# Kernel optimization log

Measured on AMD Instinct MI355X. Metric: run time of the kernel, lower is better.

## Reference

```python
import jax, jax.numpy as jnp
import numpy as np

TOPK = 1024
C = 32
FC0 = 256
EPS_BN = 1e-5
EPS_NORM = 1e-12


def setup_inputs() -> dict:
    key = jax.random.key(0)
    ks = jax.random.split(key, 8)
    B, L = 128, 16384
    N = B * L
    x = jax.random.normal(ks[0], (N, C), dtype=jnp.float32)
    length = jnp.full((B,), L, dtype=jnp.int32)
    # conv1d_1: Conv1d(32, 1, 1) -> weight [1, 32, 1] ~ vector [32], bias [1]
    w_att = jax.random.normal(ks[1], (C,), dtype=jnp.float32) * (1.0 / np.sqrt(C))
    b_att = jnp.zeros((1,), dtype=jnp.float32)
    # bn_1: BatchNorm1d(1) (eval mode: use running stats)
    g1 = jnp.ones((1,), dtype=jnp.float32)
    be1 = jnp.zeros((1,), dtype=jnp.float32)
    rm1 = jnp.zeros((1,), dtype=jnp.float32)
    rv1 = jnp.ones((1,), dtype=jnp.float32)
    # fc_1: Linear(TOPK*C, FC0)
    fan_in = TOPK * C
    W_fc = jax.random.normal(ks[2], (FC0, fan_in), dtype=jnp.float32) * (1.0 / np.sqrt(fan_in))
    b_fc = jnp.zeros((FC0,), dtype=jnp.float32)
    # bn_2: BatchNorm1d(FC0) (eval mode)
    g2 = jnp.ones((FC0,), dtype=jnp.float32)
    be2 = jnp.zeros((FC0,), dtype=jnp.float32)
    rm2 = jnp.zeros((FC0,), dtype=jnp.float32)
    rv2 = jnp.ones((FC0,), dtype=jnp.float32)
    return {"x": x, "length": length, "w_att": w_att, "b_att": b_att,
            "g1": g1, "be1": be1, "rm1": rm1, "rv1": rv1,
            "W_fc": W_fc, "b_fc": b_fc,
            "g2": g2, "be2": be2, "rm2": rm2, "rv2": rv2}


def reference(x, length, w_att, b_att, g1, be1, rm1, rv1, W_fc, b_fc, g2, be2, rm2, rv2):
    B = length.shape[0]
    N = x.shape[0]
    L = N // B  # equal-length segments (sum(length) == N)
    # attention score: 1x1 conv over channels + BatchNorm1d(1) (eval)
    att = x @ w_att + b_att[0]                                   # [N]
    att = (att - rm1[0]) * (g1[0] / jnp.sqrt(rv1[0] + EPS_BN)) + be1[0]
    # per-segment descending sort + take top TOPK == top_k per segment
    att_b = att.reshape(B, L)                                    # [B, L]
    x_b = x.reshape(B, L, C)                                     # [B, L, C]
    _, idx = jax.lax.top_k(att_b, TOPK)                          # [B, TOPK]
    ranked = jnp.take_along_axis(x_b, idx[:, :, None], axis=1)   # [B, TOPK, C]
    flat = ranked.reshape(B, TOPK * C)                           # [B, TOPK*C]
    # fc_1 + bn_2 (eval) + L2 row-normalize
    out = flat @ W_fc.T + b_fc                                   # [B, FC0]
    out = (out - rm2) * (g2 / jnp.sqrt(rv2 + EPS_BN)) + be2
    nrm = jnp.maximum(jnp.linalg.norm(out, axis=1, keepdims=True), EPS_NORM)
    return out / nrm
```

## Files before the change

kernel.cpp:

```cpp
#include <hip/hip_runtime.h>
#include <stdint.h>

#define CC 32
#define TOPK 1024
#define FC0 256
#define HL 8192

typedef __attribute__((ext_vector_type(8))) short bf16x8;
typedef __attribute__((ext_vector_type(4))) float f32x4;

__device__ __forceinline__ ushort f2bf(float f) {
    uint32_t u = __float_as_uint(f);
    uint32_t r = u + 0x7FFFu + ((u >> 16) & 1u);
    return (ushort)(r >> 16);
}

__device__ __forceinline__ uint64_t cex(uint64_t v, int s, bool up, int t)
{
    uint64_t o = (uint64_t)__shfl_xor((unsigned long long)v, s, 64);
    bool left = ((t & s) == 0);
    uint64_t mn = v < o ? v : o;
    uint64_t mx = v < o ? o : v;
    return (left == up) ? mn : mx;
}

__global__ __launch_bounds__(256)
void k_att(const float* __restrict__ x,
           const float* __restrict__ w_att, const float* __restrict__ b_att,
           uint32_t* __restrict__ key, int N)
{
    __shared__ float tile[256][CC + 1];
    const int t = threadIdx.x;
    const size_t base = (size_t)blockIdx.x * 256;
    const float4* xv = (const float4*)(x + base * CC);
    #pragma unroll
    for (int i = 0; i < 8; ++i) {
        int e = i * 256 + t;
        float4 v = xv[e];
        int r = e >> 3, c4 = (e & 7) * 4;
        tile[r][c4 + 0] = v.x; tile[r][c4 + 1] = v.y;
        tile[r][c4 + 2] = v.z; tile[r][c4 + 3] = v.w;
    }
    __syncthreads();
    float p[8];
    #pragma unroll
    for (int j = 0; j < 8; ++j) {
        float pj = __fmul_rn(tile[t][j], w_att[j]);
        pj = __fmaf_rn(tile[t][8 + j],  w_att[8 + j],  pj);
        pj = __fmaf_rn(tile[t][16 + j], w_att[16 + j], pj);
        pj = __fmaf_rn(tile[t][24 + j], w_att[24 + j], pj);
        p[j] = pj;
    }
    float q0 = __fadd_rn(p[0], p[1]);
    float q1 = __fadd_rn(p[2], p[3]);
    float q2 = __fadd_rn(p[4], p[5]);
    float q3 = __fadd_rn(p[6], p[7]);
    float dot = __fadd_rn(__fadd_rn(q0, q1), __fadd_rn(q2, q3));
    float v = __fadd_rn(dot, b_att[0]);
    uint32_t bits = __float_as_uint(v);
    key[base + t] = (bits & 0x80000000u) ? ~bits : (bits | 0x80000000u);
}

__global__ __launch_bounds__(1024)
void k_halfsel(const uint32_t* __restrict__ key, uint64_t* __restrict__ cand)
{
    __shared__ uint32_t kv[HL];
    __shared__ uint64_t cv[2048];
    __shared__ uint32_t hist[257];
    __shared__ uint32_t s_prefix, s_k, s_cnt;
    const int t = threadIdx.x;
    const int b = blockIdx.x;
    const int lane = t & 63;
    const uint32_t halfbase = (uint32_t)(b & 1) * HL;

    {
        const uint4* ks = (const uint4*)(key + (size_t)b * HL);
        uint4 a = ks[t], c = ks[t + 1024];
        *(uint4*)&kv[t * 4] = a;
        *(uint4*)&kv[(t + 1024) * 4] = c;
    }
    if (t == 0) { s_prefix = 0; s_k = TOPK; s_cnt = 0; }
    __syncthreads();

    #pragma unroll
    for (int round = 0; round < 2; ++round) {
        if (t < 257) hist[t] = 0;
        __syncthreads();
        const uint32_t pref = s_prefix;
        const uint32_t k = s_k;
        for (int i = t; i < HL; i += 1024) {
            uint32_t u = kv[i];
            if (round == 0) atomicAdd(&hist[u >> 24], 1u);
            else if ((u >> 24) == pref) atomicAdd(&hist[(u >> 16) & 255u], 1u);
        }
        __syncthreads();
        if (t < 64) {
            int l = t;
            uint32_t h0 = hist[4*l], h1 = hist[4*l+1], h2 = hist[4*l+2], h3 = hist[4*l+3];
            uint32_t s3 = h3, s2 = h2 + s3, s1 = h1 + s2, s0 = h0 + s1;
            uint32_t tot = s0, run = tot;
            #pragma unroll
            for (int off = 1; off < 64; off <<= 1) {
                int src = l + off < 64 ? l + off : 63;
                uint32_t o = __shfl(run, src, 64);
                if (l + off < 64) run += o;
            }
            uint32_t esuf = run - tot;
            hist[4*l]   = s0 + esuf; hist[4*l+1] = s1 + esuf;
            hist[4*l+2] = s2 + esuf; hist[4*l+3] = s3 + esuf;
        }
        __syncthreads();
        if (t < 256) {
            uint32_t st = hist[t], sn = hist[t + 1];
            if (st >= k && sn < k) {
                s_prefix = (pref << 8) | (uint32_t)t;
                s_k = k - sn;
            }
        }
        __syncthreads();
    }
    const uint32_t T = s_prefix << 16;

    for (int i = t; i < HL; i += 1024) {
        bool q = kv[i] >= T;
        unsigned long long m = __ballot(q);
        uint32_t base = 0;
        if (lane == 0 && m)
            base = atomicAdd(&s_cnt, (uint32_t)__popcll(m));
        base = __shfl(base, 0);
        if (q) {
            uint32_t pos = base + (uint32_t)__popcll(m & ((1ULL << lane) - 1ULL));
            if (pos < 2048)
                cv[pos] = ((uint64_t)kv[i] << 32)
                        | (uint64_t)(uint32_t)(~(halfbase + (uint32_t)i));
        }
    }
    __syncthreads();
    const uint32_t mm = s_cnt < 2048u ? s_cnt : 2048u;
    for (int i = t; i < 2048; i += 1024)
        if ((uint32_t)i >= mm) cv[i] = 0ULL;
    __syncthreads();

    {
        uint64_t r0 = cv[t], r1 = cv[t + 1024];
        #pragma unroll
        for (int size = 2; size <= 64; size <<= 1) {
            bool up = ((t & size) == 0);
            #pragma unroll
            for (int s = size >> 1; s > 0; s >>= 1) {
                r0 = cex(r0, s, up, t);
                r1 = cex(r1, s, up, t);
            }
        }
        cv[t] = r0; cv[t + 1024] = r1;
    }
    #pragma unroll
    for (int size = 128; size <= 2048; size <<= 1) {
        for (int s = size >> 1; s >= 64; s >>= 1) {
            __syncthreads();
            int i = ((t & ~(s - 1)) << 1) | (t & (s - 1));
            int j = i | s;
            uint64_t va = cv[i], vb = cv[j];
            bool up = ((i & size) == 0);
            if (up ? (va > vb) : (va < vb)) { cv[i] = vb; cv[j] = va; }
        }
        __syncthreads();
        {
            uint64_t a0 = cv[t], a1 = cv[t + 1024];
            bool up0, up1;
            if (size <= 512)      { up0 = ((t & size) == 0); up1 = up0; }
            else if (size == 1024){ up0 = true;  up1 = false; }
            else                  { up0 = true;  up1 = true;  }
            #pragma unroll
            for (int s = 32; s > 0; s >>= 1) {
                a0 = cex(a0, s, up0, t);
                a1 = cex(a1, s, up1, t);
            }
            cv[t] = a0; cv[t + 1024] = a1;
        }
        __syncthreads();
    }
    cand[(size_t)b * TOPK + t] = cv[2047 - t];
}

__global__ __launch_bounds__(1024)
void k_merge(const uint64_t* __restrict__ cand, int* __restrict__ idx_out)
{
    __shared__ uint64_t cv[2048];
    const int t = threadIdx.x;
    const int seg = blockIdx.x;
    cv[t]        = cand[(size_t)(seg * 2) * TOPK + t];
    cv[1024 + t] = cand[(size_t)(seg * 2 + 1) * TOPK + (1023 - t)];
    __syncthreads();
    for (int s = 1024; s >= 1; s >>= 1) {
        int i = ((t & ~(s - 1)) << 1) | (t & (s - 1));
        int j = i | s;
        uint64_t va = cv[i], vb = cv[j];
        if (va < vb) { cv[i] = vb; cv[j] = va; }
        __syncthreads();
    }
    idx_out[(size_t)seg * TOPK + t] = (int)(~(uint32_t)cv[t]);
}

#define NKC 128
#define KCHUNK 256

__global__ __launch_bounds__(256)
void k_fc(const float* __restrict__ x, const int* __restrict__ idx,
          const float* __restrict__ W, float* __restrict__ part, int L)
{
    __shared__ ushort flA[128][40];
    const int t = threadIdx.x;
    const int w = t >> 6;
    const int l = t & 63;
    const int l15 = l & 15;
    const int lq = l >> 4;
    const int kc = blockIdx.x;
    const int fb = blockIdx.y * 64;

    f32x4 acc[8];
    #pragma unroll
    for (int mi = 0; mi < 8; ++mi) acc[mi] = (f32x4){0.f, 0.f, 0.f, 0.f};

    const int b_ld = t >> 1, half = t & 1;
    const float* Wrow = W + (size_t)(fb + w * 16 + l15) * (TOPK * CC);

    for (int sub = 0; sub < 8; ++sub) {
        const int kbase = kc * KCHUNK + sub * 32;
        const int t_idx = kbase >> 5;
        {
            int row = idx[b_ld * TOPK + t_idx];
            row = row < 0 ? 0 : (row >= L ? L - 1 : row);
            const float4* src = (const float4*)(x + ((size_t)b_ld * L + row) * CC + half * 16);
            ushort* dst = &flA[b_ld][half * 16];
            #pragma unroll
            for (int q = 0; q < 4; ++q) {
                float4 v = src[q];
                *(uint32_t*)(dst + q * 4)     = (uint32_t)f2bf(v.x) | ((uint32_t)f2bf(v.y) << 16);
                *(uint32_t*)(dst + q * 4 + 2) = (uint32_t)f2bf(v.z) | ((uint32_t)f2bf(v.w) << 16);
            }
        }
        bf16x8 bfrag;
        {
            const float* wp = Wrow + kbase + lq * 8;
            float4 w0 = ((const float4*)wp)[0];
            float4 w1 = ((const float4*)wp)[1];
            bfrag[0] = (short)f2bf(w0.x); bfrag[1] = (short)f2bf(w0.y);
            bfrag[2] = (short)f2bf(w0.z); bfrag[3] = (short)f2bf(w0.w);
            bfrag[4] = (short)f2bf(w1.x); bfrag[5] = (short)f2bf(w1.y);
            bfrag[6] = (short)f2bf(w1.z); bfrag[7] = (short)f2bf(w1.w);
        }
        __syncthreads();
        #pragma unroll
        for (int mi = 0; mi < 8; ++mi) {
            bf16x8 afrag = *(const bf16x8*)&flA[mi * 16 + l15][lq * 8];
            acc[mi] = __builtin_amdgcn_mfma_f32_16x16x32_bf16(afrag, bfrag, acc[mi], 0, 0, 0);
        }
        __syncthreads();
    }
    float* pb = part + ((size_t)kc * 128) * 256 + fb + w * 16 + l15;
    #pragma unroll
    for (int mi = 0; mi < 8; ++mi) {
        const int brow0 = mi * 16 + lq * 4;
        #pragma unroll
        for (int r = 0; r < 4; ++r)
            pb[(size_t)(brow0 + r) * 256] = acc[mi][r];
    }
}

__global__ __launch_bounds__(256)
void k_post(const float* __restrict__ part, const float* __restrict__ b_fc,
            const float* __restrict__ g2, const float* __restrict__ be2,
            const float* __restrict__ rm2, const float* __restrict__ rv2,
            float* __restrict__ out)
{
    __shared__ float red[256];
    const int b = blockIdx.x, f = threadIdx.x;
    float s = 0.f;
    #pragma unroll 8
    for (int kc = 0; kc < NKC; ++kc)
        s += part[((size_t)kc * 128 + b) * 256 + f];
    s += b_fc[f];
    float o = (s - rm2[f]) * (g2[f] / sqrtf(rv2[f] + 1e-5f)) + be2[f];
    red[f] = o * o;
    __syncthreads();
    for (int st = 128; st > 0; st >>= 1) {
        if (f < st) red[f] += red[f + st];
        __syncthreads();
    }
    float nrm = fmaxf(sqrtf(red[0]), 1e-12f);
    out[(size_t)b * 256 + f] = o / nrm;
}

extern "C" void kernel_launch(void* const* d_in, const int* in_sizes, int n_in,
                              void* d_out, int out_size, void* d_ws, size_t ws_size,
                              hipStream_t stream)
{
    const float* x     = (const float*)d_in[0];
    const float* w_att = (const float*)d_in[2];
    const float* b_att = (const float*)d_in[3];
    const float* W_fc  = (const float*)d_in[8];
    const float* b_fc  = (const float*)d_in[9];
    const float* g2    = (const float*)d_in[10];
    const float* be2   = (const float*)d_in[11];
    const float* rm2   = (const float*)d_in[12];
    const float* rv2   = (const float*)d_in[13];

    const int N = in_sizes[0] / CC;
    const int B = in_sizes[1];
    const int L = N / B;

    const size_t off_key  = 0;
    const size_t off_cand = off_key + (size_t)N * 4;
    const size_t off_idx  = off_cand + (size_t)2 * B * TOPK * 8;
    const size_t off_part = off_idx + (size_t)B * TOPK * 4;

    uint8_t* ws = (uint8_t*)d_ws;
    uint32_t* key  = (uint32_t*)(ws + off_key);
    uint64_t* cand = (uint64_t*)(ws + off_cand);
    int* idx       = (int*)(ws + off_idx);
    float* part    = (float*)(ws + off_part);

    k_att<<<N / 256, 256, 0, stream>>>(x, w_att, b_att, key, N);
    k_halfsel<<<2 * B, 1024, 0, stream>>>(key, cand);
    k_merge<<<B, 1024, 0, stream>>>(cand, idx);
    dim3 g3(NKC, FC0 / 64);
    k_fc<<<g3, 256, 0, stream>>>(x, idx, W_fc, part, L);
    k_post<<<B, 256, 0, stream>>>(part, b_fc, g2, be2, rm2, rv2, (float*)d_out);
}
```

Before: 105.3 us.

## Fuse per-segment top-k into one kernel with register keys and rank-by-count

Replaces the two-half radix select plus bitonic sort and the separate bitonic merge kernel with a single kernel per segment. Each thread keeps its 16 keys in registers, runs the two-round radix histogram to find the threshold, and compacts about TOPK candidates into shared memory. Each candidate's output position is then found by counting how many candidates are larger, an O(cnt²) broadcast scan. This removes a kernel launch, the global candidate round trip and the many barrier-separated sort stages. In exchange, only B blocks run instead of 2B, and the quadratic rank loop could be slow when many candidates pass the threshold.

```diff
diff --git a/kernel.cpp b/kernel.cpp
--- a/kernel.cpp
+++ b/kernel.cpp
@@ -4,7 +4,7 @@
 #define CC 32
 #define TOPK 1024
 #define FC0 256
-#define HL 8192
+#define SL 16384
 
 typedef __attribute__((ext_vector_type(8))) short bf16x8;
 typedef __attribute__((ext_vector_type(4))) float f32x4;
@@ -13,15 +13,6 @@
     uint32_t u = __float_as_uint(f);
     uint32_t r = u + 0x7FFFu + ((u >> 16) & 1u);
     return (ushort)(r >> 16);
-}
-
-__device__ __forceinline__ uint64_t cex(uint64_t v, int s, bool up, int t)
-{
-    uint64_t o = (uint64_t)__shfl_xor((unsigned long long)v, s, 64);
-    bool left = ((t & s) == 0);
-    uint64_t mn = v < o ? v : o;
-    uint64_t mx = v < o ? o : v;
-    return (left == up) ? mn : mx;
 }
 
 __global__ __launch_bounds__(256)
@@ -62,22 +53,24 @@
 }
 
 __global__ __launch_bounds__(1024)
-void k_halfsel(const uint32_t* __restrict__ key, uint64_t* __restrict__ cand)
-{
-    __shared__ uint32_t kv[HL];
+void k_topk(const uint32_t* __restrict__ key, int* __restrict__ idx_out)
+{
     __shared__ uint64_t cv[2048];
     __shared__ uint32_t hist[257];
     __shared__ uint32_t s_prefix, s_k, s_cnt;
     const int t = threadIdx.x;
-    const int b = blockIdx.x;
+    const int seg = blockIdx.x;
     const int lane = t & 63;
-    const uint32_t halfbase = (uint32_t)(b & 1) * HL;
-
+
+    uint32_t rk[16];
     {
-        const uint4* ks = (const uint4*)(key + (size_t)b * HL);
-        uint4 a = ks[t], c = ks[t + 1024];
-        *(uint4*)&kv[t * 4] = a;
-        *(uint4*)&kv[(t + 1024) * 4] = c;
+        const uint4* ks = (const uint4*)(key + (size_t)seg * SL);
+        #pragma unroll
+        for (int q = 0; q < 4; ++q) {
+            uint4 a = ks[t + q * 1024];
+            rk[q * 4 + 0] = a.x; rk[q * 4 + 1] = a.y;
+            rk[q * 4 + 2] = a.z; rk[q * 4 + 3] = a.w;
+        }
     }
     if (t == 0) { s_prefix = 0; s_k = TOPK; s_cnt = 0; }
     __syncthreads();
@@ -88,8 +81,9 @@
         __syncthreads();
         const uint32_t pref = s_prefix;
         const uint32_t k = s_k;
-        for (int i = t; i < HL; i += 1024) {
-            uint32_t u = kv[i];
+        #pragma unroll
+        for (int q = 0; q < 16; ++q) {
+            uint32_t u = rk[q];
             if (round == 0) atomicAdd(&hist[u >> 24], 1u);
             else if ((u >> 24) == pref) atomicAdd(&hist[(u >> 16) & 255u], 1u);
         }
@@ -121,85 +115,32 @@
     }
     const uint32_t T = s_prefix << 16;
 
-    for (int i = t; i < HL; i += 1024) {
-        bool q = kv[i] >= T;
-        unsigned long long m = __ballot(q);
+    #pragma unroll
+    for (int q = 0; q < 16; ++q) {
+        bool qq = rk[q] >= T;
+        unsigned long long m = __ballot(qq);
         uint32_t base = 0;
         if (lane == 0 && m)
             base = atomicAdd(&s_cnt, (uint32_t)__popcll(m));
         base = __shfl(base, 0);
-        if (q) {
+        if (qq) {
+            uint32_t idx = 4u * t + (q & 3) + (uint32_t)(q >> 2) * 4096u;
             uint32_t pos = base + (uint32_t)__popcll(m & ((1ULL << lane) - 1ULL));
             if (pos < 2048)
-                cv[pos] = ((uint64_t)kv[i] << 32)
-                        | (uint64_t)(uint32_t)(~(halfbase + (uint32_t)i));
-        }
-    }
-    __syncthreads();
-    const uint32_t mm = s_cnt < 2048u ? s_cnt : 2048u;
-    for (int i = t; i < 2048; i += 1024)
-        if ((uint32_t)i >= mm) cv[i] = 0ULL;
-    __syncthreads();
-
-    {
-        uint64_t r0 = cv[t], r1 = cv[t + 1024];
-        #pragma unroll
-        for (int size = 2; size <= 64; size <<= 1) {
-            bool up = ((t & size) == 0);
-            #pragma unroll
-            for (int s = size >> 1; s > 0; s >>= 1) {
-                r0 = cex(r0, s, up, t);
-                r1 = cex(r1, s, up, t);
-            }
-        }
-        cv[t] = r0; cv[t + 1024] = r1;
-    }
-    #pragma unroll
-    for (int size = 128; size <= 2048; size <<= 1) {
-        for (int s = size >> 1; s >= 64; s >>= 1) {
-            __syncthreads();
-            int i = ((t & ~(s - 1)) << 1) | (t & (s - 1));
-            int j = i | s;
-            uint64_t va = cv[i], vb = cv[j];
-            bool up = ((i & size) == 0);
-            if (up ? (va > vb) : (va < vb)) { cv[i] = vb; cv[j] = va; }
-        }
-        __syncthreads();
-        {
-            uint64_t a0 = cv[t], a1 = cv[t + 1024];
-            bool up0, up1;
-            if (size <= 512)      { up0 = ((t & size) == 0); up1 = up0; }
-            else if (size == 1024){ up0 = true;  up1 = false; }
-            else                  { up0 = true;  up1 = true;  }
-            #pragma unroll
-            for (int s = 32; s > 0; s >>= 1) {
-                a0 = cex(a0, s, up0, t);
-                a1 = cex(a1, s, up1, t);
-            }
-            cv[t] = a0; cv[t + 1024] = a1;
-        }
-        __syncthreads();
-    }
-    cand[(size_t)b * TOPK + t] = cv[2047 - t];
-}
-
-__global__ __launch_bounds__(1024)
-void k_merge(const uint64_t* __restrict__ cand, int* __restrict__ idx_out)
-{
-    __shared__ uint64_t cv[2048];
-    const int t = threadIdx.x;
-    const int seg = blockIdx.x;
-    cv[t]        = cand[(size_t)(seg * 2) * TOPK + t];
-    cv[1024 + t] = cand[(size_t)(seg * 2 + 1) * TOPK + (1023 - t)];
-    __syncthreads();
-    for (int s = 1024; s >= 1; s >>= 1) {
-        int i = ((t & ~(s - 1)) << 1) | (t & (s - 1));
-        int j = i | s;
-        uint64_t va = cv[i], vb = cv[j];
-        if (va < vb) { cv[i] = vb; cv[j] = va; }
-        __syncthreads();
-    }
-    idx_out[(size_t)seg * TOPK + t] = (int)(~(uint32_t)cv[t]);
+                cv[pos] = ((uint64_t)rk[q] << 32) | (uint64_t)(uint32_t)(~idx);
+        }
+    }
+    __syncthreads();
+    const uint32_t cnt = s_cnt < 2048u ? s_cnt : 2048u;
+
+    for (uint32_t i = t; i < cnt; i += 1024) {
+        const uint64_t my = cv[i];
+        uint32_t r = 0;
+        for (uint32_t j = 0; j < cnt; ++j)
+            r += (cv[j] > my) ? 1u : 0u;
+        if (r < TOPK)
+            idx_out[(size_t)seg * TOPK + r] = (int)(~(uint32_t)my);
+    }
 }
 
 #define NKC 128
@@ -309,21 +250,19 @@
     const int N = in_sizes[0] / CC;
     const int B = in_sizes[1];
     const int L = N / B;
+    (void)L;
 
     const size_t off_key  = 0;
-    const size_t off_cand = off_key + (size_t)N * 4;
-    const size_t off_idx  = off_cand + (size_t)2 * B * TOPK * 8;
+    const size_t off_idx  = off_key + (size_t)N * 4;
     const size_t off_part = off_idx + (size_t)B * TOPK * 4;
 
     uint8_t* ws = (uint8_t*)d_ws;
     uint32_t* key  = (uint32_t*)(ws + off_key);
-    uint64_t* cand = (uint64_t*)(ws + off_cand);
     int* idx       = (int*)(ws + off_idx);
     float* part    = (float*)(ws + off_part);
 
     k_att<<<N / 256, 256, 0, stream>>>(x, w_att, b_att, key, N);
-    k_halfsel<<<2 * B, 1024, 0, stream>>>(key, cand);
-    k_merge<<<B, 1024, 0, stream>>>(cand, idx);
+    k_topk<<<B, 1024, 0, stream>>>(key, idx);
     dim3 g3(NKC, FC0 / 64);
     k_fc<<<g3, 256, 0, stream>>>(x, idx, W_fc, part, L);
     k_post<<<B, 256, 0, stream>>>(part, b_fc, g2, be2, rm2, rv2, (float*)d_out);
```

Result: slower. 120.0 us (+14.0%).
